# Kernel optimization log

Hardware: AMD Instinct MI355X
Metric: run time of the kernel (lower is better)

The kernel has to match this reference:

```python
import jax, jax.numpy as jnp
import numpy as np

EMBED_DIM = 768
HIDDEN = 768


def setup_inputs() -> dict:
    key = jax.random.key(0)
    k1, k2, k3, k4 = jax.random.split(key, 4)
    doc_embed = jax.random.normal(k1, (32, 1024, EMBED_DIM), dtype=jnp.float32)
    query_embed = jax.random.normal(k2, (32, 128, EMBED_DIM), dtype=jnp.float32)
    # nn.Linear params: weight [H, E], bias [H]
    bound = 1.0 / np.sqrt(EMBED_DIM)
    W = jax.random.uniform(k3, (HIDDEN, EMBED_DIM), minval=-bound, maxval=bound, dtype=jnp.float32)
    b = jax.random.uniform(k4, (HIDDEN,), minval=-bound, maxval=bound, dtype=jnp.float32)
    return {"doc_embed": doc_embed, "query_embed": query_embed, "W": W, "b": b}


def reference(doc_embed, query_embed, W, b):
    # shared linear projection + ReLU
    doc_o = jax.nn.relu(jnp.einsum('bde,he->bdh', doc_embed, W) + b)    # [B, Ld, H]
    query_o = jax.nn.relu(jnp.einsum('bqe,he->bqh', query_embed, W) + b)  # [B, Lq, H]
    # unscaled cross-attention scores over query positions
    scores = jnp.einsum('bdh,bqh->bdq', doc_o, query_o)  # [B, Ld, Lq]
    attn = jax.nn.softmax(scores, axis=-1)
    out = jnp.einsum('bdq,bqe->bde', attn, query_embed)  # [B, Ld, E]
    return out
```

## Files before the change

### kernel.cpp

```cpp
#include <hip/hip_runtime.h>

typedef _Float16 f16x8 __attribute__((ext_vector_type(8)));
typedef float f32x4 __attribute__((ext_vector_type(4)));

#define EMB 768
#define LQ 128
#define LD 1024
#define NB 32

typedef const __attribute__((address_space(1))) char gas_char;
typedef __attribute__((address_space(3))) char las_char;

__device__ __forceinline__ void gload16(const void* g, void* l) {
    __builtin_amdgcn_global_load_lds((gas_char*)g, (las_char*)l, 16, 0, 0);
}

#define SWZ(row, ch) ((row) * 64 + ((((ch) ^ ((row) & 7))) * 8))

#define BAR() asm volatile("s_barrier" ::: "memory")
#define LGKM0() do { asm volatile("s_waitcnt lgkmcnt(0)" ::: "memory"); \
                     __builtin_amdgcn_sched_barrier(0); } while (0)
#define VMW(N) asm volatile("s_waitcnt vmcnt(" #N ")" ::: "memory")

__global__ void cvt8_kernel(const float* __restrict__ in, _Float16* __restrict__ out, int n8) {
    int i = blockIdx.x * 256 + threadIdx.x;
    if (i >= n8) return;
    const float4 a = ((const float4*)in)[2 * i];
    const float4 b = ((const float4*)in)[2 * i + 1];
    f16x8 o;
    o[0] = (_Float16)a.x; o[1] = (_Float16)a.y; o[2] = (_Float16)a.z; o[3] = (_Float16)a.w;
    o[4] = (_Float16)b.x; o[5] = (_Float16)b.y; o[6] = (_Float16)b.z; o[7] = (_Float16)b.w;
    ((f16x8*)out)[i] = o;
}

__global__ void make_vt_kernel(const float* __restrict__ Q, _Float16* __restrict__ VT) {
    int i = blockIdx.x * 256 + threadIdx.x;
    if (i >= NB * EMB * LQ) return;
    int q = i % LQ;
    int e = (i / LQ) % EMB;
    int b = i / (LQ * EMB);
    VT[i] = (_Float16)Q[((size_t)b * LQ + q) * EMB + e];
}

__device__ __forceinline__ void stage_tile(const _Float16* g, _Float16* l, int tid) {
#pragma unroll
    for (int i = 0; i < 4; ++i) {
        const int idx = i * 256 + tid;
        const int row = idx >> 3, ch = idx & 7;
        gload16(g + (size_t)row * EMB + ((ch ^ (row & 7)) * 8), l + (size_t)idx * 8);
    }
}

__global__ __launch_bounds__(512, 2) void proj8_kernel(
    const _Float16* __restrict__ A, const _Float16* __restrict__ W16,
    const float* __restrict__ bias, _Float16* __restrict__ OUT) {
    extern __shared__ _Float16 smem[];
    const int tid = threadIdx.x, wave = tid >> 6, lane = tid & 63;
    const int lr = lane & 15, lkg = lane >> 4;
    const int wr = wave >> 2, wc = wave & 3;

    const int nwg = gridDim.x, cpx = nwg >> 3;
    const int swz = (blockIdx.x & 7) * cpx + (blockIdx.x >> 3);
    const int rowblk = swz / 3, colblk = swz - rowblk * 3;
    const int row0 = rowblk * 256, col0 = colblk * 256;

    const int r0_ = tid >> 3, c0_ = (((tid & 7) ^ (r0_ & 7)) * 8);
    const int r1_ = (512 + tid) >> 3, c1_ = ((((512 + tid) & 7) ^ (r1_ & 7)) * 8);
    const int lo0 = tid * 8, lo1 = (512 + tid) * 8;

    const _Float16* gA0 = A + (size_t)row0 * EMB;
    const _Float16* gA1 = A + (size_t)(row0 + 128) * EMB;
    const _Float16* gB0 = W16 + (size_t)col0 * EMB;
    const _Float16* gB1 = W16 + (size_t)(col0 + 128) * EMB;

#define STAGE_PAIR(g0, g1, kt, lbase) do { \
    const _Float16* s0_ = (g0) + (kt) * 64; const _Float16* s1_ = (g1) + (kt) * 64; \
    _Float16* d_ = (lbase); \
    gload16(s0_ + (size_t)r0_ * EMB + c0_, d_ + lo0); \
    gload16(s0_ + (size_t)r1_ * EMB + c1_, d_ + lo1); \
    gload16(s1_ + (size_t)r0_ * EMB + c0_, d_ + 8192 + lo0); \
    gload16(s1_ + (size_t)r1_ * EMB + c1_, d_ + 8192 + lo1); } while (0)

    f32x4 acc[8][4];
#pragma unroll
    for (int m = 0; m < 8; ++m)
#pragma unroll
        for (int n = 0; n < 4; ++n) acc[m][n] = (f32x4){0.f, 0.f, 0.f, 0.f};

    f16x8 aF[4][2], bF[4][2];
    const int bro = (wc & 1) * 64;

#define READ_A(slot, MH) do { _Float16* ab_ = smem + (slot) * 32768 + wr * 8192; \
    _Pragma("unroll") for (int mm = 0; mm < 4; ++mm) _Pragma("unroll") for (int ks = 0; ks < 2; ++ks) \
        aF[mm][ks] = *(const f16x8*)(ab_ + SWZ(((MH) * 4 + mm) * 16 + lr, ks * 4 + lkg)); } while (0)
#define READ_B(slot, NH) do { _Float16* bb_ = smem + (slot) * 32768 + 16384 + (wc >> 1) * 8192; \
    _Pragma("unroll") for (int nn = 0; nn < 2; ++nn) _Pragma("unroll") for (int ks = 0; ks < 2; ++ks) \
        bF[(NH) * 2 + nn][ks] = *(const f16x8*)(bb_ + SWZ(bro + ((NH) * 2 + nn) * 16 + lr, ks * 4 + lkg)); } while (0)
#define MFMA_Q(MH, NH) do { __builtin_amdgcn_s_setprio(1); \
    _Pragma("unroll") for (int mm = 0; mm < 4; ++mm) _Pragma("unroll") for (int nn = 0; nn < 2; ++nn) \
    _Pragma("unroll") for (int ks = 0; ks < 2; ++ks) \
        acc[(MH) * 4 + mm][(NH) * 2 + nn] = __builtin_amdgcn_mfma_f32_16x16x32_f16( \
            aF[mm][ks], bF[(NH) * 2 + nn][ks], acc[(MH) * 4 + mm][(NH) * 2 + nn], 0, 0, 0); \
    __builtin_amdgcn_s_setprio(0); } while (0)

    STAGE_PAIR(gB0, gB1, 0, smem + 16384);
    STAGE_PAIR(gA0, gA1, 0, smem);
    STAGE_PAIR(gB0, gB1, 1, smem + 32768 + 16384);
    STAGE_PAIR(gA0, gA1, 1, smem + 32768);
    VMW(8);
    BAR();

#pragma unroll 1
    for (int j = 0; j < 6; ++j) {
        const int kt2 = 2 * j + 2, kt3 = 2 * j + 3;
        READ_B(0, 0); READ_B(0, 1); READ_A(0, 0);
        BAR(); LGKM0(); MFMA_Q(0, 0); BAR();
        BAR(); LGKM0(); MFMA_Q(0, 1); BAR();
        READ_A(0, 1);
        if (j < 5) STAGE_PAIR(gB0, gB1, kt2, smem + 16384);
        BAR(); LGKM0(); MFMA_Q(1, 0); BAR();
        if (j < 5) { STAGE_PAIR(gA0, gA1, kt2, smem); VMW(4); }
        else       { VMW(0); }
        BAR(); LGKM0(); MFMA_Q(1, 1); BAR();
        READ_B(1, 0); READ_B(1, 1); READ_A(1, 0);
        BAR(); LGKM0(); MFMA_Q(0, 0); BAR();
        BAR(); LGKM0(); MFMA_Q(0, 1); BAR();
        READ_A(1, 1);
        if (j < 5) STAGE_PAIR(gB0, gB1, kt3, smem + 32768 + 16384);
        BAR(); LGKM0(); MFMA_Q(1, 0); BAR();
        if (j < 5) { STAGE_PAIR(gA0, gA1, kt3, smem + 32768); VMW(4); }
        BAR(); LGKM0(); MFMA_Q(1, 1); BAR();
    }

    const int crow = lkg * 4;
#pragma unroll
    for (int n = 0; n < 4; ++n) {
        const int gc = col0 + wc * 64 + n * 16 + lr;
        const float bv = bias[gc];
#pragma unroll
        for (int m = 0; m < 8; ++m) {
            const size_t gr = (size_t)row0 + wr * 128 + m * 16 + crow;
#pragma unroll
            for (int r = 0; r < 4; ++r) {
                float v = acc[m][n][r] + bv;
                OUT[(gr + r) * EMB + gc] = (_Float16)(v > 0.f ? v : 0.f);
            }
        }
    }
#undef STAGE_PAIR
#undef READ_A
#undef READ_B
#undef MFMA_Q
}

__global__ __launch_bounds__(256) void attn128_kernel(
    const _Float16* __restrict__ Do, const _Float16* __restrict__ Qo,
    const _Float16* __restrict__ VT, float* __restrict__ OUT) {
    __shared__ __align__(16) _Float16 smem[32768];
    const int tid = threadIdx.x, wave = tid >> 6, lane = tid & 63;
    const int lr = lane & 15, lkg = lane >> 4;
    const int b = blockIdx.x, dblk = blockIdx.y;
    const _Float16* gd = Do + ((size_t)b * LD + dblk * 128) * EMB;
    const _Float16* gq = Qo + (size_t)b * LQ * EMB;

    f32x4 s[2][8];
#pragma unroll
    for (int m = 0; m < 2; ++m)
#pragma unroll
        for (int n = 0; n < 8; ++n) s[m][n] = (f32x4){0.f, 0.f, 0.f, 0.f};

    stage_tile(gd, smem, tid);
    stage_tile(gq, smem + 8192, tid);
    int cur = 0;
    for (int it = 0; it < 12; ++it) {
        __syncthreads();
        if (it < 11) {
            stage_tile(gd + (it + 1) * 64, smem + (cur ^ 1) * 16384, tid);
            stage_tile(gq + (it + 1) * 64, smem + (cur ^ 1) * 16384 + 8192, tid);
        }
        const _Float16* sD = smem + cur * 16384;
        const _Float16* sQ = sD + 8192;
#pragma unroll
        for (int kk = 0; kk < 2; ++kk) {
            const int ch = kk * 4 + lkg;
            f16x8 am[2];
#pragma unroll
            for (int m = 0; m < 2; ++m)
                am[m] = *(const f16x8*)(sD + SWZ(wave * 32 + m * 16 + lr, ch));
#pragma unroll
            for (int n = 0; n < 8; ++n) {
                const f16x8 bq = *(const f16x8*)(sQ + SWZ(n * 16 + lr, ch));
#pragma unroll
                for (int m = 0; m < 2; ++m)
                    s[m][n] = __builtin_amdgcn_mfma_f32_16x16x32_f16(am[m], bq, s[m][n], 0, 0, 0);
            }
        }
        cur ^= 1;
    }
    __syncthreads();

    _Float16 (*P)[136] = (_Float16 (*)[136])smem;
    const int crow = lkg * 4;
#pragma unroll
    for (int m = 0; m < 2; ++m) {
#pragma unroll
        for (int r = 0; r < 4; ++r) {
            float mx = -1e30f;
#pragma unroll
            for (int n = 0; n < 8; ++n) mx = fmaxf(mx, s[m][n][r]);
#pragma unroll
            for (int off = 1; off < 16; off <<= 1) mx = fmaxf(mx, __shfl_xor(mx, off));
            float p[8], sum = 0.f;
#pragma unroll
            for (int n = 0; n < 8; ++n) { p[n] = __expf(s[m][n][r] - mx); sum += p[n]; }
#pragma unroll
            for (int off = 1; off < 16; off <<= 1) sum += __shfl_xor(sum, off);
            const float inv = 1.f / sum;
            const int row = wave * 32 + m * 16 + crow + r;
#pragma unroll
            for (int n = 0; n < 8; ++n) P[row][n * 16 + lr] = (_Float16)(p[n] * inv);
        }
    }
    __syncthreads();

    const _Float16* vtb = VT + (size_t)b * EMB * LQ;
#pragma unroll 1
    for (int nc = 0; nc < 6; ++nc) {
        f32x4 o[2][8];
#pragma unroll
        for (int m = 0; m < 2; ++m)
#pragma unroll
            for (int t = 0; t < 8; ++t) o[m][t] = (f32x4){0.f, 0.f, 0.f, 0.f};
#pragma unroll
        for (int ks = 0; ks < 4; ++ks) {
            f16x8 am[2];
#pragma unroll
            for (int m = 0; m < 2; ++m)
                am[m] = *(const f16x8*)(&P[wave * 32 + m * 16 + lr][ks * 32 + lkg * 8]);
#pragma unroll
            for (int t = 0; t < 8; ++t) {
                const f16x8 bv = *(const f16x8*)(vtb + (size_t)(nc * 128 + t * 16 + lr) * LQ + ks * 32 + lkg * 8);
#pragma unroll
                for (int m = 0; m < 2; ++m)
                    o[m][t] = __builtin_amdgcn_mfma_f32_16x16x32_f16(am[m], bv, o[m][t], 0, 0, 0);
            }
        }
#pragma unroll
        for (int t = 0; t < 8; ++t) {
#pragma unroll
            for (int m = 0; m < 2; ++m) {
                const size_t gr = (size_t)b * LD + dblk * 128 + wave * 32 + m * 16 + crow;
                const int e = nc * 128 + t * 16 + lr;
#pragma unroll
                for (int r = 0; r < 4; ++r)
                    OUT[(gr + r) * EMB + e] = o[m][t][r];
            }
        }
    }
}

extern "C" void kernel_launch(void* const* d_in, const int* in_sizes, int n_in,
                              void* d_out, int out_size, void* d_ws, size_t ws_size,
                              hipStream_t stream) {
    const float* doc   = (const float*)d_in[0];
    const float* query = (const float*)d_in[1];
    const float* W     = (const float*)d_in[2];
    const float* bias  = (const float*)d_in[3];
    float* out = (float*)d_out;

    const size_t nW  = (size_t)EMB * EMB;
    const size_t nVT = (size_t)NB * EMB * LQ;
    const size_t nDo = (size_t)NB * LD * EMB;
    const size_t nQo = (size_t)NB * LQ * EMB;
    const size_t need = (nW + nVT + nDo + nQo) * sizeof(_Float16);
    if (ws_size < need) return;

    _Float16* W16 = (_Float16*)d_ws;
    _Float16* VT  = W16 + nW;
    _Float16* Do  = VT + nVT;
    _Float16* Qo  = Do + nDo;

    _Float16* doc16 = (_Float16*)d_out;
    _Float16* q16   = doc16 + nDo;

    cvt8_kernel<<<(int)(nDo / 8 / 256), 256, 0, stream>>>(doc, doc16, (int)(nDo / 8));
    cvt8_kernel<<<(int)(nQo / 8 / 256), 256, 0, stream>>>(query, q16, (int)(nQo / 8));
    cvt8_kernel<<<(int)(nW / 8 / 256), 256, 0, stream>>>(W, W16, (int)(nW / 8));
    make_vt_kernel<<<(int)(nVT / 256), 256, 0, stream>>>(query, VT);

    hipFuncSetAttribute(reinterpret_cast<const void*>(&proj8_kernel),
                        hipFuncAttributeMaxDynamicSharedMemorySize, 131072);
    proj8_kernel<<<dim3(144 * 3), 512, 131072, stream>>>(doc16, W16, bias, Do);

    attn128_kernel<<<dim3(NB, LD / 128), 256, 0, stream>>>(Do, Qo, VT, out);
}
```

Before: 154.6 us.

## Fuse fp32-to-fp16 activation conversion into projection GEMM A-tile loading

```diff
diff --git a/kernel.cpp b/kernel.cpp
--- a/kernel.cpp
+++ b/kernel.cpp
@@ -51,9 +51,10 @@
     }
 }
 
-__global__ __launch_bounds__(512, 2) void proj8_kernel(
-    const _Float16* __restrict__ A, const _Float16* __restrict__ W16,
-    const float* __restrict__ bias, _Float16* __restrict__ OUT) {
+__global__ __launch_bounds__(512, 2) void proj8f_kernel(
+    const float* __restrict__ doc, const float* __restrict__ query,
+    const _Float16* __restrict__ W16, const float* __restrict__ bias,
+    _Float16* __restrict__ OUT) {
     extern __shared__ _Float16 smem[];
     const int tid = threadIdx.x, wave = tid >> 6, lane = tid & 63;
     const int lr = lane & 15, lkg = lane >> 4;
@@ -61,81 +62,101 @@
 
     const int nwg = gridDim.x, cpx = nwg >> 3;
     const int swz = (blockIdx.x & 7) * cpx + (blockIdx.x >> 3);
-    const int rowblk = swz / 3, colblk = swz - rowblk * 3;
-    const int row0 = rowblk * 256, col0 = colblk * 256;
-
-    const int r0_ = tid >> 3, c0_ = (((tid & 7) ^ (r0_ & 7)) * 8);
-    const int r1_ = (512 + tid) >> 3, c1_ = ((((512 + tid) & 7) ^ (r1_ & 7)) * 8);
-    const int lo0 = tid * 8, lo1 = (512 + tid) * 8;
-
-    const _Float16* gA0 = A + (size_t)row0 * EMB;
-    const _Float16* gA1 = A + (size_t)(row0 + 128) * EMB;
-    const _Float16* gB0 = W16 + (size_t)col0 * EMB;
-    const _Float16* gB1 = W16 + (size_t)(col0 + 128) * EMB;
-
-#define STAGE_PAIR(g0, g1, kt, lbase) do { \
-    const _Float16* s0_ = (g0) + (kt) * 64; const _Float16* s1_ = (g1) + (kt) * 64; \
-    _Float16* d_ = (lbase); \
-    gload16(s0_ + (size_t)r0_ * EMB + c0_, d_ + lo0); \
-    gload16(s0_ + (size_t)r1_ * EMB + c1_, d_ + lo1); \
-    gload16(s1_ + (size_t)r0_ * EMB + c0_, d_ + 8192 + lo0); \
-    gload16(s1_ + (size_t)r1_ * EMB + c1_, d_ + 8192 + lo1); } while (0)
-
-    f32x4 acc[8][4];
+    const int rowblk = swz / 6, colblk = swz - rowblk * 6;
+    const int row0 = rowblk * 256, col0 = colblk * 128;
+
+    const float* gAf = (rowblk < 128) ? doc + (size_t)row0 * EMB
+                                      : query + (size_t)(row0 - 32768) * EMB;
+    const _Float16* gB = W16 + (size_t)col0 * EMB;
+
+    int arow[4], ach[4];
+#pragma unroll
+    for (int w = 0; w < 4; ++w) {
+        const int cidx = w * 512 + tid;
+        arow[w] = cidx >> 3; ach[w] = cidx & 7;
+    }
+    int brow[2], bch[2];
+#pragma unroll
+    for (int w = 0; w < 2; ++w) {
+        const int idx = w * 512 + tid;
+        brow[w] = idx >> 3; bch[w] = idx & 7;
+    }
+
+#define ISSUE_A(kt, f) do { _Pragma("unroll") for (int w_ = 0; w_ < 4; ++w_) { \
+        const float* s_ = gAf + (size_t)arow[w_] * EMB + (kt) * 64 + ach[w_] * 8; \
+        f[w_][0] = *(const float4*)s_; f[w_][1] = *(const float4*)(s_ + 4); } } while (0)
+
+#define WRITE_A(slot, f) do { _Pragma("unroll") for (int w_ = 0; w_ < 4; ++w_) { \
+        f16x8 v_; \
+        v_[0] = (_Float16)f[w_][0].x; v_[1] = (_Float16)f[w_][0].y; \
+        v_[2] = (_Float16)f[w_][0].z; v_[3] = (_Float16)f[w_][0].w; \
+        v_[4] = (_Float16)f[w_][1].x; v_[5] = (_Float16)f[w_][1].y; \
+        v_[6] = (_Float16)f[w_][1].z; v_[7] = (_Float16)f[w_][1].w; \
+        const int half_ = arow[w_] >> 7, lrow_ = arow[w_] & 127; \
+        *(f16x8*)(smem + (slot) * 16384 + half_ * 8192 + SWZ(lrow_, ach[w_])) = v_; } } while (0)
+
+#define STAGE_B(kt, slot) do { _Pragma("unroll") for (int w_ = 0; w_ < 2; ++w_) \
+        gload16(gB + (size_t)brow[w_] * EMB + (kt) * 64 + ((bch[w_] ^ (brow[w_] & 7)) * 8), \
+                smem + 32768 + (slot) * 8192 + (size_t)(w_ * 512 + tid) * 8); } while (0)
+
+    f32x4 acc[8][2];
 #pragma unroll
     for (int m = 0; m < 8; ++m)
 #pragma unroll
-        for (int n = 0; n < 4; ++n) acc[m][n] = (f32x4){0.f, 0.f, 0.f, 0.f};
-
-    f16x8 aF[4][2], bF[4][2];
-    const int bro = (wc & 1) * 64;
-
-#define READ_A(slot, MH) do { _Float16* ab_ = smem + (slot) * 32768 + wr * 8192; \
+        for (int n = 0; n < 2; ++n) acc[m][n] = (f32x4){0.f, 0.f, 0.f, 0.f};
+
+    f16x8 aF[4][2], bF[2][2];
+
+#define READ_A(slot, MH) do { const _Float16* ab_ = smem + (slot) * 16384 + wr * 8192; \
     _Pragma("unroll") for (int mm = 0; mm < 4; ++mm) _Pragma("unroll") for (int ks = 0; ks < 2; ++ks) \
         aF[mm][ks] = *(const f16x8*)(ab_ + SWZ(((MH) * 4 + mm) * 16 + lr, ks * 4 + lkg)); } while (0)
-#define READ_B(slot, NH) do { _Float16* bb_ = smem + (slot) * 32768 + 16384 + (wc >> 1) * 8192; \
+#define READ_B(slot) do { const _Float16* bb_ = smem + 32768 + (slot) * 8192; \
     _Pragma("unroll") for (int nn = 0; nn < 2; ++nn) _Pragma("unroll") for (int ks = 0; ks < 2; ++ks) \
-        bF[(NH) * 2 + nn][ks] = *(const f16x8*)(bb_ + SWZ(bro + ((NH) * 2 + nn) * 16 + lr, ks * 4 + lkg)); } while (0)
-#define MFMA_Q(MH, NH) do { __builtin_amdgcn_s_setprio(1); \
+        bF[nn][ks] = *(const f16x8*)(bb_ + SWZ(wc * 32 + nn * 16 + lr, ks * 4 + lkg)); } while (0)
+#define MFMA_H(MH) do { __builtin_amdgcn_s_setprio(1); \
     _Pragma("unroll") for (int mm = 0; mm < 4; ++mm) _Pragma("unroll") for (int nn = 0; nn < 2; ++nn) \
     _Pragma("unroll") for (int ks = 0; ks < 2; ++ks) \
-        acc[(MH) * 4 + mm][(NH) * 2 + nn] = __builtin_amdgcn_mfma_f32_16x16x32_f16( \
-            aF[mm][ks], bF[(NH) * 2 + nn][ks], acc[(MH) * 4 + mm][(NH) * 2 + nn], 0, 0, 0); \
+        acc[(MH) * 4 + mm][nn] = __builtin_amdgcn_mfma_f32_16x16x32_f16( \
+            aF[mm][ks], bF[nn][ks], acc[(MH) * 4 + mm][nn], 0, 0, 0); \
     __builtin_amdgcn_s_setprio(0); } while (0)
 
-    STAGE_PAIR(gB0, gB1, 0, smem + 16384);
-    STAGE_PAIR(gA0, gA1, 0, smem);
-    STAGE_PAIR(gB0, gB1, 1, smem + 32768 + 16384);
-    STAGE_PAIR(gA0, gA1, 1, smem + 32768);
-    VMW(8);
+    float4 fA[4][2], fA2[4][2];
+
+    ISSUE_A(0, fA);
+    STAGE_B(0, 0);
+    VMW(2);
+    WRITE_A(0, fA);
+    ISSUE_A(1, fA2);
+    STAGE_B(1, 1);
+    VMW(2);
+    asm volatile("s_waitcnt lgkmcnt(0)" ::: "memory");
     BAR();
 
 #pragma unroll 1
     for (int j = 0; j < 6; ++j) {
         const int kt2 = 2 * j + 2, kt3 = 2 * j + 3;
-        READ_B(0, 0); READ_B(0, 1); READ_A(0, 0);
-        BAR(); LGKM0(); MFMA_Q(0, 0); BAR();
-        BAR(); LGKM0(); MFMA_Q(0, 1); BAR();
+        WRITE_A(1, fA2);
+        if (j < 5) { ISSUE_A(kt2, fA); ISSUE_A(kt3, fA2); }
+        READ_B(0); READ_A(0, 0);
+        BAR(); LGKM0(); MFMA_H(0); BAR();
         READ_A(0, 1);
-        if (j < 5) STAGE_PAIR(gB0, gB1, kt2, smem + 16384);
-        BAR(); LGKM0(); MFMA_Q(1, 0); BAR();
-        if (j < 5) { STAGE_PAIR(gA0, gA1, kt2, smem); VMW(4); }
+        if (j < 5) { STAGE_B(kt2, 0); VMW(18); }
         else       { VMW(0); }
-        BAR(); LGKM0(); MFMA_Q(1, 1); BAR();
-        READ_B(1, 0); READ_B(1, 1); READ_A(1, 0);
-        BAR(); LGKM0(); MFMA_Q(0, 0); BAR();
-        BAR(); LGKM0(); MFMA_Q(0, 1); BAR();
+        BAR(); LGKM0(); MFMA_H(1); BAR();
+        VMW(10);
+        if (j < 5) WRITE_A(0, fA);
+        READ_B(1); READ_A(1, 0);
+        BAR(); LGKM0(); MFMA_H(0); BAR();
         READ_A(1, 1);
-        if (j < 5) STAGE_PAIR(gB0, gB1, kt3, smem + 32768 + 16384);
-        BAR(); LGKM0(); MFMA_Q(1, 0); BAR();
-        if (j < 5) { STAGE_PAIR(gA0, gA1, kt3, smem + 32768); VMW(4); }
-        BAR(); LGKM0(); MFMA_Q(1, 1); BAR();
+        if (j < 5) STAGE_B(kt3, 1);
+        VMW(2);
+        BAR(); LGKM0(); MFMA_H(1); BAR();
     }
 
     const int crow = lkg * 4;
 #pragma unroll
-    for (int n = 0; n < 4; ++n) {
-        const int gc = col0 + wc * 64 + n * 16 + lr;
+    for (int n = 0; n < 2; ++n) {
+        const int gc = col0 + wc * 32 + n * 16 + lr;
         const float bv = bias[gc];
 #pragma unroll
         for (int m = 0; m < 8; ++m) {
@@ -147,10 +168,12 @@
             }
         }
     }
-#undef STAGE_PAIR
+#undef ISSUE_A
+#undef WRITE_A
+#undef STAGE_B
 #undef READ_A
 #undef READ_B
-#undef MFMA_Q
+#undef MFMA_H
 }
 
 __global__ __launch_bounds__(256) void attn128_kernel(
@@ -280,17 +303,12 @@
     _Float16* Do  = VT + nVT;
     _Float16* Qo  = Do + nDo;
 
-    _Float16* doc16 = (_Float16*)d_out;
-    _Float16* q16   = doc16 + nDo;
-
-    cvt8_kernel<<<(int)(nDo / 8 / 256), 256, 0, stream>>>(doc, doc16, (int)(nDo / 8));
-    cvt8_kernel<<<(int)(nQo / 8 / 256), 256, 0, stream>>>(query, q16, (int)(nQo / 8));
     cvt8_kernel<<<(int)(nW / 8 / 256), 256, 0, stream>>>(W, W16, (int)(nW / 8));
     make_vt_kernel<<<(int)(nVT / 256), 256, 0, stream>>>(query, VT);
 
-    hipFuncSetAttribute(reinterpret_cast<const void*>(&proj8_kernel),
-                        hipFuncAttributeMaxDynamicSharedMemorySize, 131072);
-    proj8_kernel<<<dim3(144 * 3), 512, 131072, stream>>>(doc16, W16, bias, Do);
+    hipFuncSetAttribute(reinterpret_cast<const void*>(&proj8f_kernel),
+                        hipFuncAttributeMaxDynamicSharedMemorySize, 98304);
+    proj8f_kernel<<<dim3(144 * 6), 512, 98304, stream>>>(doc, query, W16, bias, Do);
 
     attn128_kernel<<<dim3(NB, LD / 128), 256, 0, stream>>>(Do, Qo, VT, out);
 }
```

Measured after the change: 174.1 us. +12.6%, slower.

## Transpose VT via LDS tiles and shrink attention tile to 64 doc rows

Applied to the files above, without the earlier changes.

```diff
diff --git a/kernel.cpp b/kernel.cpp
--- a/kernel.cpp
+++ b/kernel.cpp
@@ -1,6 +1,7 @@
 #include <hip/hip_runtime.h>
 
 typedef _Float16 f16x8 __attribute__((ext_vector_type(8)));
+typedef _Float16 f16x4 __attribute__((ext_vector_type(4)));
 typedef float f32x4 __attribute__((ext_vector_type(4)));
 
 #define EMB 768
@@ -33,18 +34,41 @@
     ((f16x8*)out)[i] = o;
 }
 
-__global__ void make_vt_kernel(const float* __restrict__ Q, _Float16* __restrict__ VT) {
-    int i = blockIdx.x * 256 + threadIdx.x;
-    if (i >= NB * EMB * LQ) return;
-    int q = i % LQ;
-    int e = (i / LQ) % EMB;
-    int b = i / (LQ * EMB);
-    VT[i] = (_Float16)Q[((size_t)b * LQ + q) * EMB + e];
+__global__ __launch_bounds__(256) void make_vt_kernel(const float* __restrict__ Q,
+                                                      _Float16* __restrict__ VT) {
+    __shared__ float t[64][65];
+    const int tid = threadIdx.x;
+    const int q0 = blockIdx.x * 64, e0 = blockIdx.y * 64, b = blockIdx.z;
+    const int rr = tid >> 4, cc = (tid & 15) * 4;
+#pragma unroll
+    for (int i = 0; i < 4; ++i) {
+        const int row = i * 16 + rr;
+        const float4 v = *(const float4*)(Q + ((size_t)b * LQ + q0 + row) * EMB + e0 + cc);
+        t[row][cc + 0] = v.x; t[row][cc + 1] = v.y; t[row][cc + 2] = v.z; t[row][cc + 3] = v.w;
+    }
+    __syncthreads();
+#pragma unroll
+    for (int i = 0; i < 4; ++i) {
+        const int erow = i * 16 + rr;
+        f16x4 v;
+#pragma unroll
+        for (int j = 0; j < 4; ++j) v[j] = (_Float16)t[cc + j][erow];
+        *(f16x4*)(VT + ((size_t)b * EMB + e0 + erow) * LQ + q0 + cc) = v;
+    }
 }
 
 __device__ __forceinline__ void stage_tile(const _Float16* g, _Float16* l, int tid) {
 #pragma unroll
     for (int i = 0; i < 4; ++i) {
+        const int idx = i * 256 + tid;
+        const int row = idx >> 3, ch = idx & 7;
+        gload16(g + (size_t)row * EMB + ((ch ^ (row & 7)) * 8), l + (size_t)idx * 8);
+    }
+}
+
+__device__ __forceinline__ void stage_d64(const _Float16* g, _Float16* l, int tid) {
+#pragma unroll
+    for (int i = 0; i < 2; ++i) {
         const int idx = i * 256 + tid;
         const int row = idx >> 3, ch = idx & 7;
         gload16(g + (size_t)row * EMB + ((ch ^ (row & 7)) * 8), l + (size_t)idx * 8);
@@ -153,46 +177,43 @@
 #undef MFMA_Q
 }
 
-__global__ __launch_bounds__(256) void attn128_kernel(
+__global__ __launch_bounds__(256) void attn64_kernel(
     const _Float16* __restrict__ Do, const _Float16* __restrict__ Qo,
     const _Float16* __restrict__ VT, float* __restrict__ OUT) {
-    __shared__ __align__(16) _Float16 smem[32768];
+    __shared__ __align__(16) _Float16 smem[24576];
     const int tid = threadIdx.x, wave = tid >> 6, lane = tid & 63;
     const int lr = lane & 15, lkg = lane >> 4;
-    const int b = blockIdx.x, dblk = blockIdx.y;
-    const _Float16* gd = Do + ((size_t)b * LD + dblk * 128) * EMB;
+
+    const int l = blockIdx.x;
+    const int x = l & 7, i = l >> 3;
+    const int b = x * 4 + (i >> 4), dblk = i & 15;
+
+    const _Float16* gd = Do + ((size_t)b * LD + dblk * 64) * EMB;
     const _Float16* gq = Qo + (size_t)b * LQ * EMB;
 
-    f32x4 s[2][8];
-#pragma unroll
-    for (int m = 0; m < 2; ++m)
-#pragma unroll
-        for (int n = 0; n < 8; ++n) s[m][n] = (f32x4){0.f, 0.f, 0.f, 0.f};
-
-    stage_tile(gd, smem, tid);
-    stage_tile(gq, smem + 8192, tid);
+    f32x4 s[8];
+#pragma unroll
+    for (int n = 0; n < 8; ++n) s[n] = (f32x4){0.f, 0.f, 0.f, 0.f};
+
+    stage_d64(gd, smem, tid);
+    stage_tile(gq, smem + 4096, tid);
     int cur = 0;
     for (int it = 0; it < 12; ++it) {
         __syncthreads();
         if (it < 11) {
-            stage_tile(gd + (it + 1) * 64, smem + (cur ^ 1) * 16384, tid);
-            stage_tile(gq + (it + 1) * 64, smem + (cur ^ 1) * 16384 + 8192, tid);
-        }
-        const _Float16* sD = smem + cur * 16384;
-        const _Float16* sQ = sD + 8192;
+            stage_d64(gd + (it + 1) * 64, smem + (cur ^ 1) * 12288, tid);
+            stage_tile(gq + (it + 1) * 64, smem + (cur ^ 1) * 12288 + 4096, tid);
+        }
+        const _Float16* sD = smem + cur * 12288;
+        const _Float16* sQ = sD + 4096;
 #pragma unroll
         for (int kk = 0; kk < 2; ++kk) {
             const int ch = kk * 4 + lkg;
-            f16x8 am[2];
-#pragma unroll
-            for (int m = 0; m < 2; ++m)
-                am[m] = *(const f16x8*)(sD + SWZ(wave * 32 + m * 16 + lr, ch));
+            const f16x8 am = *(const f16x8*)(sD + SWZ(wave * 16 + lr, ch));
 #pragma unroll
             for (int n = 0; n < 8; ++n) {
                 const f16x8 bq = *(const f16x8*)(sQ + SWZ(n * 16 + lr, ch));
-#pragma unroll
-                for (int m = 0; m < 2; ++m)
-                    s[m][n] = __builtin_amdgcn_mfma_f32_16x16x32_f16(am[m], bq, s[m][n], 0, 0, 0);
+                s[n] = __builtin_amdgcn_mfma_f32_16x16x32_f16(am, bq, s[n], 0, 0, 0);
             }
         }
         cur ^= 1;
@@ -202,59 +223,47 @@
     _Float16 (*P)[136] = (_Float16 (*)[136])smem;
     const int crow = lkg * 4;
 #pragma unroll
-    for (int m = 0; m < 2; ++m) {
-#pragma unroll
-        for (int r = 0; r < 4; ++r) {
-            float mx = -1e30f;
-#pragma unroll
-            for (int n = 0; n < 8; ++n) mx = fmaxf(mx, s[m][n][r]);
-#pragma unroll
-            for (int off = 1; off < 16; off <<= 1) mx = fmaxf(mx, __shfl_xor(mx, off));
-            float p[8], sum = 0.f;
-#pragma unroll
-            for (int n = 0; n < 8; ++n) { p[n] = __expf(s[m][n][r] - mx); sum += p[n]; }
-#pragma unroll
-            for (int off = 1; off < 16; off <<= 1) sum += __shfl_xor(sum, off);
-            const float inv = 1.f / sum;
-            const int row = wave * 32 + m * 16 + crow + r;
-#pragma unroll
-            for (int n = 0; n < 8; ++n) P[row][n * 16 + lr] = (_Float16)(p[n] * inv);
-        }
+    for (int r = 0; r < 4; ++r) {
+        float mx = -1e30f;
+#pragma unroll
+        for (int n = 0; n < 8; ++n) mx = fmaxf(mx, s[n][r]);
+#pragma unroll
+        for (int off = 1; off < 16; off <<= 1) mx = fmaxf(mx, __shfl_xor(mx, off));
+        float p[8], sum = 0.f;
+#pragma unroll
+        for (int n = 0; n < 8; ++n) { p[n] = __expf(s[n][r] - mx); sum += p[n]; }
+#pragma unroll
+        for (int off = 1; off < 16; off <<= 1) sum += __shfl_xor(sum, off);
+        const float inv = 1.f / sum;
+        const int row = wave * 16 + crow + r;
+#pragma unroll
+        for (int n = 0; n < 8; ++n) P[row][n * 16 + lr] = (_Float16)(p[n] * inv);
     }
     __syncthreads();
 
     const _Float16* vtb = VT + (size_t)b * EMB * LQ;
+    const size_t dbase = (size_t)b * LD + dblk * 64 + wave * 16 + crow;
 #pragma unroll 1
     for (int nc = 0; nc < 6; ++nc) {
-        f32x4 o[2][8];
-#pragma unroll
-        for (int m = 0; m < 2; ++m)
-#pragma unroll
-            for (int t = 0; t < 8; ++t) o[m][t] = (f32x4){0.f, 0.f, 0.f, 0.f};
+        f32x4 o[8];
+#pragma unroll
+        for (int t = 0; t < 8; ++t) o[t] = (f32x4){0.f, 0.f, 0.f, 0.f};
 #pragma unroll
         for (int ks = 0; ks < 4; ++ks) {
-            f16x8 am[2];
-#pragma unroll
-            for (int m = 0; m < 2; ++m)
-                am[m] = *(const f16x8*)(&P[wave * 32 + m * 16 + lr][ks * 32 + lkg * 8]);
+            const f16x8 am = *(const f16x8*)(&P[wave * 16 + lr][ks * 32 + lkg * 8]);
 #pragma unroll
             for (int t = 0; t < 8; ++t) {
-                const f16x8 bv = *(const f16x8*)(vtb + (size_t)(nc * 128 + t * 16 + lr) * LQ + ks * 32 + lkg * 8);
-#pragma unroll
-                for (int m = 0; m < 2; ++m)
-                    o[m][t] = __builtin_amdgcn_mfma_f32_16x16x32_f16(am[m], bv, o[m][t], 0, 0, 0);
+                const f16x8 bv = *(const f16x8*)(vtb + (size_t)(nc * 128 + t * 16 + lr) * LQ
+                                                 + ks * 32 + lkg * 8);
+                o[t] = __builtin_amdgcn_mfma_f32_16x16x32_f16(am, bv, o[t], 0, 0, 0);
             }
         }
 #pragma unroll
         for (int t = 0; t < 8; ++t) {
-#pragma unroll
-            for (int m = 0; m < 2; ++m) {
-                const size_t gr = (size_t)b * LD + dblk * 128 + wave * 32 + m * 16 + crow;
-                const int e = nc * 128 + t * 16 + lr;
-#pragma unroll
-                for (int r = 0; r < 4; ++r)
-                    OUT[(gr + r) * EMB + e] = o[m][t][r];
-            }
+            const int e = nc * 128 + t * 16 + lr;
+#pragma unroll
+            for (int r = 0; r < 4; ++r)
+                OUT[(dbase + r) * EMB + e] = o[t][r];
         }
     }
 }
@@ -286,11 +295,11 @@
     cvt8_kernel<<<(int)(nDo / 8 / 256), 256, 0, stream>>>(doc, doc16, (int)(nDo / 8));
     cvt8_kernel<<<(int)(nQo / 8 / 256), 256, 0, stream>>>(query, q16, (int)(nQo / 8));
     cvt8_kernel<<<(int)(nW / 8 / 256), 256, 0, stream>>>(W, W16, (int)(nW / 8));
-    make_vt_kernel<<<(int)(nVT / 256), 256, 0, stream>>>(query, VT);
+    make_vt_kernel<<<dim3(2, 12, NB), 256, 0, stream>>>(query, VT);
 
     hipFuncSetAttribute(reinterpret_cast<const void*>(&proj8_kernel),
                         hipFuncAttributeMaxDynamicSharedMemorySize, 131072);
     proj8_kernel<<<dim3(144 * 3), 512, 131072, stream>>>(doc16, W16, bias, Do);
 
-    attn128_kernel<<<dim3(NB, LD / 128), 256, 0, stream>>>(Do, Qo, VT, out);
-}
+    attn64_kernel<<<dim3(NB * 16), 256, 0, stream>>>(Do, Qo, VT, out);
+}
```

After: 150.8 us. 2.5% less time.
